# Optimization experiments

Measured on AMD Instinct MI355X. Metric: run time of the kernel, lower is better.

The kernel has to match this reference:

```python
import jax, jax.numpy as jnp
import numpy as np
import math

B, DG, P, DA = 512, 1024, 1024, 256
LN_EPS = 1e-5  # torch LayerNorm default
EPS = 1e-12


def _ln(x, g, b):
    mu = jnp.mean(x, axis=-1, keepdims=True)
    var = jnp.mean((x - mu) ** 2, axis=-1, keepdims=True)
    return (x - mu) * jax.lax.rsqrt(var + LN_EPS) * g + b


def setup_inputs() -> dict:
    key = jax.random.key(0)
    ks = jax.random.split(key, 16)
    s = lambda fan_in: 1.0 / math.sqrt(fan_in)
    return {
        "hg": jax.random.normal(ks[0], (B, DG), jnp.float32),
        "desc_2d": jax.random.normal(ks[1], (B, P), jnp.float32),
        "Wq": jax.random.uniform(ks[2], (DA, DG), jnp.float32, -s(DG), s(DG)),
        "bq": jnp.zeros((DA,), jnp.float32),
        "wk_val": jax.random.uniform(ks[3], (DA,), jnp.float32, -1.0, 1.0),
        "bk_val": jax.random.uniform(ks[4], (DA,), jnp.float32, -1.0, 1.0),
        "wv_val": jax.random.uniform(ks[5], (DA,), jnp.float32, -1.0, 1.0),
        "bv_val": jax.random.uniform(ks[6], (DA,), jnp.float32, -1.0, 1.0),
        "Ek": jax.random.normal(ks[7], (P, DA), jnp.float32),
        "Ev": jax.random.normal(ks[8], (P, DA), jnp.float32),
        "Uq": jax.random.uniform(ks[9], (DA, DA), jnp.float32, -s(DA), s(DA)),
        "Vk": jax.random.uniform(ks[10], (DA, DA), jnp.float32, -s(DA), s(DA)),
        "ln_q_g": jnp.ones((DA,), jnp.float32), "ln_q_b": jnp.zeros((DA,), jnp.float32),
        "ln_k_g": jnp.ones((DA,), jnp.float32), "ln_k_b": jnp.zeros((DA,), jnp.float32),
        "ln_v_g": jnp.ones((DA,), jnp.float32), "ln_v_b": jnp.zeros((DA,), jnp.float32),
    }


def reference(hg, desc_2d, Wq, bq, wk_val, bk_val, wv_val, bv_val, Ek, Ev, Uq, Vk,
              ln_q_g, ln_q_b, ln_k_g, ln_k_b, ln_v_g, ln_v_b):
    # dropout is inference-mode (identity)
    q = _ln(hg @ Wq.T + bq, ln_q_g, ln_q_b)                       # (B, DA)
    # scalar -> token proj plus id embedding
    k = desc_2d[:, :, None] * wk_val + bk_val + Ek[None]          # (B, P, DA)
    v = desc_2d[:, :, None] * wv_val + bv_val + Ev[None]
    k = _ln(k, ln_k_g, ln_k_b)
    v = _ln(v, ln_v_g, ln_v_b)
    q2 = q @ Uq.T                                                 # (B, DA)
    k2 = jnp.einsum('bpd,ed->bpe', k, Vk)                         # (B, P, DA)
    e = jnp.einsum('bpd,bd->bp', k2, q2) / math.sqrt(DA)          # (B, P)
    alpha = jax.nn.sigmoid(e)
    alpha = alpha / (jnp.sum(alpha, axis=1, keepdims=True) + EPS)
    c = jnp.einsum('bp,bpd->bd', alpha, v)                        # (B, DA)
    return c, alpha
```

## Files before the change

kernel.cpp:

```cpp
#include <hip/hip_runtime.h>
#include <math.h>

#define B 512
#define DG 1024
#define P 1024
#define DA 256
#define LDP 68
#define BP (B * P)
#define BD (B * DA)

__device__ __forceinline__ float block_reduce_sum(float v, volatile float* red) {
    #pragma unroll
    for (int off = 32; off > 0; off >>= 1) v += __shfl_down(v, off, 64);
    const int lane = threadIdx.x & 63, wid = threadIdx.x >> 6;
    __syncthreads();
    if (lane == 0) red[wid] = v;
    __syncthreads();
    return red[0] + red[1] + red[2] + red[3];
}
__device__ __forceinline__ float wsum(float v) {
    #pragma unroll
    for (int m = 32; m > 0; m >>= 1) v += __shfl_xor(v, m, 64);
    return v;
}

#define FMA16(a4, b4, acc)                                   \
    acc[0][0] = fmaf(a4.x, b4.x, acc[0][0]);                 \
    acc[0][1] = fmaf(a4.x, b4.y, acc[0][1]);                 \
    acc[0][2] = fmaf(a4.x, b4.z, acc[0][2]);                 \
    acc[0][3] = fmaf(a4.x, b4.w, acc[0][3]);                 \
    acc[1][0] = fmaf(a4.y, b4.x, acc[1][0]);                 \
    acc[1][1] = fmaf(a4.y, b4.y, acc[1][1]);                 \
    acc[1][2] = fmaf(a4.y, b4.z, acc[1][2]);                 \
    acc[1][3] = fmaf(a4.y, b4.w, acc[1][3]);                 \
    acc[2][0] = fmaf(a4.z, b4.x, acc[2][0]);                 \
    acc[2][1] = fmaf(a4.z, b4.y, acc[2][1]);                 \
    acc[2][2] = fmaf(a4.z, b4.z, acc[2][2]);                 \
    acc[2][3] = fmaf(a4.z, b4.w, acc[2][3]);                 \
    acc[3][0] = fmaf(a4.w, b4.x, acc[3][0]);                 \
    acc[3][1] = fmaf(a4.w, b4.y, acc[3][1]);                 \
    acc[3][2] = fmaf(a4.w, b4.z, acc[3][2]);                 \
    acc[3][3] = fmaf(a4.w, b4.w, acc[3][3]);

__device__ __forceinline__ void stage_T(const float* __restrict__ src, int ldk, int m0, int k0,
                                        int tid, float* sD) {
    const int m = tid >> 3, k4 = (tid & 7) * 4;
    #pragma unroll
    for (int pass = 0; pass < 2; ++pass) {
        int mm = m + pass * 32;
        float4 v = *reinterpret_cast<const float4*>(&src[(m0 + mm) * ldk + k0 + k4]);
        sD[(k4 + 0) * LDP + mm] = v.x; sD[(k4 + 1) * LDP + mm] = v.y;
        sD[(k4 + 2) * LDP + mm] = v.z; sD[(k4 + 3) * LDP + mm] = v.w;
    }
}
__device__ __forceinline__ void stage_N1(const float* __restrict__ src, int ldn, int k0, int n0,
                                         int tid, float* sD) {
    const int k = tid >> 4, n4 = (tid & 15) * 4;
    #pragma unroll
    for (int pass = 0; pass < 2; ++pass) {
        int kk = k + pass * 16;
        *reinterpret_cast<float4*>(&sD[kk * LDP + n4]) =
            *reinterpret_cast<const float4*>(&src[(k0 + kk) * ldn + n0 + n4]);
    }
}
__device__ __forceinline__ void stage_N2(const float* __restrict__ src, int pstride, int ldn,
                                         int k0, int n0, int tid, float* sD) {
    const int k = tid >> 4, n4 = (tid & 15) * 4;
    #pragma unroll
    for (int pass = 0; pass < 2; ++pass) {
        int kk = k + pass * 16;
        const float* base = &src[(k0 + kk) * ldn + n0 + n4];
        float4 v = *reinterpret_cast<const float4*>(base);
        float4 w = *reinterpret_cast<const float4*>(base + pstride);
        v.x += w.x; v.y += w.y; v.z += w.z; v.w += w.w;
        *reinterpret_cast<float4*>(&sD[kk * LDP + n4]) = v;
    }
}
__device__ __forceinline__ void mm_inner(const float* sA, const float* sB, int tid, float acc[4][4]) {
    const int ty4 = (tid >> 4) * 4, tx4 = (tid & 15) * 4;
    #pragma unroll
    for (int kk = 0; kk < 32; ++kk) {
        float4 a4 = *reinterpret_cast<const float4*>(&sA[kk * LDP + ty4]);
        float4 b4 = *reinterpret_cast<const float4*>(&sB[kk * LDP + tx4]);
        FMA16(a4, b4, acc)
    }
}

__global__ __launch_bounds__(256) void KA(const float* __restrict__ hg, const float* __restrict__ Wq,
                                          const float* __restrict__ Uq, const float* __restrict__ Vk,
                                          const float* __restrict__ Ek, const float* __restrict__ Ev,
                                          const float* __restrict__ wk, const float* __restrict__ bk,
                                          const float* __restrict__ wv, const float* __restrict__ bv,
                                          const float* __restrict__ gk, const float* __restrict__ bkln,
                                          float* __restrict__ qp, float* __restrict__ Gp,
                                          float* __restrict__ UqT,
                                          float* __restrict__ pst, float* __restrict__ scal4,
                                          float* __restrict__ vec4) {
    __shared__ __align__(16) float sA[32 * LDP];
    __shared__ __align__(16) float sB[32 * LDP];
    const int tid = threadIdx.x, t = blockIdx.x;
    const int ty4 = (tid >> 4) * 4, tx4 = (tid & 15) * 4;

    if (t < 256) {
        const int mt = t & 7, nt = (t >> 3) & 3, ks = t >> 5;
        const int b0 = mt * 64, d0 = nt * 64, kc = ks * 128;
        float acc[4][4] = {};
        for (int kt = 0; kt < 128; kt += 32) {
            stage_T(hg, DG, b0, kc + kt, tid, sA);
            stage_T(Wq, DG, d0, kc + kt, tid, sB);
            __syncthreads();
            mm_inner(sA, sB, tid, acc);
            __syncthreads();
        }
        float* outp = qp + ks * BD;
        #pragma unroll
        for (int i = 0; i < 4; ++i) {
            float4 o = make_float4(acc[i][0], acc[i][1], acc[i][2], acc[i][3]);
            *reinterpret_cast<float4*>(&outp[(b0 + ty4 + i) * DA + d0 + tx4]) = o;
        }
    } else if (t < 384) {
        const int t2 = t - 256;
        const int et = t2 & 3, pt = (t2 >> 2) & 15, ks = t2 >> 6;
        const int e0 = et * 64, p0 = pt * 64, kc = ks * 128;
        float acc[4][4] = {};
        for (int kt = 0; kt < 128; kt += 32) {
            const int kg = kc + kt;
            {
                const int m = tid >> 3, k4 = (tid & 7) * 4;
                float4 g = *reinterpret_cast<const float4*>(&gk[kg + k4]);
                #pragma unroll
                for (int pass = 0; pass < 2; ++pass) {
                    int mm = m + pass * 32;
                    float4 v = *reinterpret_cast<const float4*>(&Vk[(e0 + mm) * DA + kg + k4]);
                    sA[(k4 + 0) * LDP + mm] = v.x * g.x; sA[(k4 + 1) * LDP + mm] = v.y * g.y;
                    sA[(k4 + 2) * LDP + mm] = v.z * g.z; sA[(k4 + 3) * LDP + mm] = v.w * g.w;
                }
            }
            stage_T(Ek, DA, p0, kg, tid, sB);
            __syncthreads();
            mm_inner(sA, sB, tid, acc);
            __syncthreads();
        }
        float* outp = Gp + ks * (DA * P);
        #pragma unroll
        for (int i = 0; i < 4; ++i) {
            float4 o = make_float4(acc[i][0], acc[i][1], acc[i][2], acc[i][3]);
            *reinterpret_cast<float4*>(&outp[(e0 + ty4 + i) * P + p0 + tx4]) = o;
        }
    } else if (t < 448) {
        const int b2 = t - 384;
        const int e0 = (b2 & 7) * 32, f0 = (b2 >> 3) * 32;
        const int col = tid & 31, row8 = tid >> 5;
        #pragma unroll
        for (int pass = 0; pass < 4; ++pass) {
            int r = row8 + pass * 8;
            sA[r * 33 + col] = Uq[(e0 + r) * DA + f0 + col];
        }
        __syncthreads();
        #pragma unroll
        for (int pass = 0; pass < 4; ++pass) {
            int r = row8 + pass * 8;
            UqT[(f0 + r) * DA + e0 + col] = sA[col * 33 + r];
        }
    } else if (t == 448) {
        float* w4  = sA;
        float* tmp = sB;
        float gkd = gk[tid];
        w4[0 * 256 + tid] = wk[tid] * gkd;
        w4[1 * 256 + tid] = bk[tid] * gkd;
        w4[2 * 256 + tid] = gkd;
        w4[3 * 256 + tid] = bkln[tid];
        __syncthreads();
        const int dl = tid & 15, eg = tid >> 4;
        for (int eb = 0; eb < 16; ++eb) {
            int e = eb * 16 + eg;
            float p0 = 0.f, p1 = 0.f, p2 = 0.f, p3 = 0.f;
            #pragma unroll
            for (int tt = 0; tt < 16; ++tt) {
                int d = dl + tt * 16;
                float v = Vk[e * DA + d];
                p0 = fmaf(v, w4[d], p0);
                p1 = fmaf(v, w4[256 + d], p1);
                p2 = fmaf(v, w4[512 + d], p2);
                p3 = fmaf(v, w4[768 + d], p3);
            }
            #pragma unroll
            for (int m = 8; m > 0; m >>= 1) {
                p0 += __shfl_xor(p0, m, 16);
                p1 += __shfl_xor(p1, m, 16);
                p2 += __shfl_xor(p2, m, 16);
                p3 += __shfl_xor(p3, m, 16);
            }
            if (dl == 0) {
                tmp[e * 4 + 0] = p0; tmp[e * 4 + 1] = p1;
                tmp[e * 4 + 2] = p2; tmp[e * 4 + 3] = p3;
            }
        }
        __syncthreads();
        float a0 = 0.f, a1 = 0.f, a2 = 0.f, a3 = 0.f;
        for (int e = 0; e < 256; ++e) {
            float u = Uq[e * DA + tid];
            a0 = fmaf(u, tmp[e * 4 + 0], a0);
            a1 = fmaf(u, tmp[e * 4 + 1], a1);
            a2 = fmaf(u, tmp[e * 4 + 2], a2);
            a3 = fmaf(u, tmp[e * 4 + 3], a3);
        }
        vec4[tid] = a0; vec4[256 + tid] = a1; vec4[512 + tid] = a2; vec4[768 + tid] = a3;
    } else {
        const int tp = t - 449;
        const int wid = tid >> 6, lane = tid & 63;
        const int p = tp * 4 + wid;
        const int d4 = lane * 4;
        const float inv = 1.0f / DA;
        float4 ek4 = *reinterpret_cast<const float4*>(&Ek[p * DA + d4]);
        float4 ev4 = *reinterpret_cast<const float4*>(&Ev[p * DA + d4]);
        float4 wk4 = *reinterpret_cast<const float4*>(&wk[d4]);
        float4 bk4 = *reinterpret_cast<const float4*>(&bk[d4]);
        float4 wv4 = *reinterpret_cast<const float4*>(&wv[d4]);
        float4 bv4 = *reinterpret_cast<const float4*>(&bv[d4]);
        float ck0 = bk4.x + ek4.x, ck1 = bk4.y + ek4.y, ck2 = bk4.z + ek4.z, ck3 = bk4.w + ek4.w;
        float cv0 = bv4.x + ev4.x, cv1 = bv4.y + ev4.y, cv2 = bv4.z + ev4.z, cv3 = bv4.w + ev4.w;
        float Sck  = wsum(ck0 + ck1 + ck2 + ck3);
        float Sck2 = wsum(ck0*ck0 + ck1*ck1 + ck2*ck2 + ck3*ck3);
        float Swck = wsum(wk4.x*ck0 + wk4.y*ck1 + wk4.z*ck2 + wk4.w*ck3);
        float Scv  = wsum(cv0 + cv1 + cv2 + cv3);
        float Scv2 = wsum(cv0*cv0 + cv1*cv1 + cv2*cv2 + cv3*cv3);
        float Swcv = wsum(wv4.x*cv0 + wv4.y*cv1 + wv4.z*cv2 + wv4.w*cv3);
        float Swk  = wsum(wk4.x + wk4.y + wk4.z + wk4.w);
        float Swv  = wsum(wv4.x + wv4.y + wv4.z + wv4.w);
        float mwk = Swk * inv, mwv = Swv * inv;
        float mck = Sck * inv, mcv = Scv * inv;
        if (lane == 0) {
            pst[0 * P + p] = mck;
            pst[1 * P + p] = Swck * inv - mwk * mck;
            pst[2 * P + p] = Sck2 * inv - mck * mck;
            pst[3 * P + p] = mcv;
            pst[4 * P + p] = Swcv * inv - mwv * mcv;
            pst[5 * P + p] = Scv2 * inv - mcv * mcv;
        }
        if (p == 0) {
            float Swk2 = wsum(wk4.x*wk4.x + wk4.y*wk4.y + wk4.z*wk4.z + wk4.w*wk4.w);
            float Swv2 = wsum(wv4.x*wv4.x + wv4.y*wv4.y + wv4.z*wv4.z + wv4.w*wv4.w);
            if (lane == 0) {
                scal4[0] = mwk;
                scal4[1] = Swk2 * inv - mwk * mwk;
                scal4[2] = mwv;
                scal4[3] = Swv2 * inv - mwv * mwv;
            }
        }
    }
}

__global__ __launch_bounds__(256) void KC(const float* __restrict__ qp, const float* __restrict__ bq,
                                          const float* __restrict__ gq, const float* __restrict__ bqln,
                                          const float* __restrict__ vec4, const float* __restrict__ UqT,
                                          float* __restrict__ q2out, float* __restrict__ bscal) {
    __shared__ __align__(16) float q_lds[DA];
    __shared__ float red[4];
    const int b = blockIdx.x, d = threadIdx.x;
    float x = bq[d];
    #pragma unroll
    for (int ks = 0; ks < 8; ++ks) x += qp[ks * BD + b * DA + d];
    float mu = block_reduce_sum(x, red) * (1.0f / DA);
    float xc = x - mu;
    float var = block_reduce_sum(xc * xc, red) * (1.0f / DA);
    float qv = xc * rsqrtf(var + 1e-5f) * gq[d] + bqln[d];
    q_lds[d] = qv;
    float Wg = block_reduce_sum(qv * vec4[d], red);
    float Cg = block_reduce_sum(qv * vec4[256 + d], red);
    float G_ = block_reduce_sum(qv * vec4[512 + d], red);
    float Bb = block_reduce_sum(qv * vec4[768 + d], red);
    if (d == 0) {
        bscal[b] = Wg; bscal[B + b] = Cg;
        bscal[2 * B + b] = G_; bscal[3 * B + b] = Bb;
    }
    float q2 = 0.f;
    for (int f = 0; f < DA; f += 4) {
        float4 qf = *reinterpret_cast<const float4*>(&q_lds[f]);
        q2 = fmaf(qf.x, UqT[(f + 0) * DA + d], q2);
        q2 = fmaf(qf.y, UqT[(f + 1) * DA + d], q2);
        q2 = fmaf(qf.z, UqT[(f + 2) * DA + d], q2);
        q2 = fmaf(qf.w, UqT[(f + 3) * DA + d], q2);
    }
    q2out[b * DA + d] = q2;
}

__global__ __launch_bounds__(256) void KD(const float* __restrict__ q2, const float* __restrict__ Gp,
                                          float* __restrict__ epart) {
    __shared__ __align__(16) float sA[32 * LDP];
    __shared__ __align__(16) float sB[32 * LDP];
    const int tid = threadIdx.x, t = blockIdx.x;
    const int ty4 = (tid >> 4) * 4, tx4 = (tid & 15) * 4;
    const int bt = t & 7, pt = (t >> 3) & 15, ks = t >> 7;
    const int b0 = bt * 64, p0 = pt * 64, kc = ks * 64;
    float acc[4][4] = {};
    for (int kt = 0; kt < 64; kt += 32) {
        stage_T(q2, DA, b0, kc + kt, tid, sA);
        stage_N2(Gp, DA * P, P, kc + kt, p0, tid, sB);
        __syncthreads();
        mm_inner(sA, sB, tid, acc);
        __syncthreads();
    }
    float* outp = epart + ks * BP;
    #pragma unroll
    for (int i = 0; i < 4; ++i) {
        float4 o = make_float4(acc[i][0], acc[i][1], acc[i][2], acc[i][3]);
        *reinterpret_cast<float4*>(&outp[(b0 + ty4 + i) * P + p0 + tx4]) = o;
    }
}

__global__ __launch_bounds__(256) void KE(const float* __restrict__ epart, const float* __restrict__ desc,
                                          const float* __restrict__ bscal, const float* __restrict__ pst,
                                          const float* __restrict__ scal4,
                                          const float* __restrict__ gv, const float* __restrict__ wv,
                                          const float* __restrict__ bvv, const float* __restrict__ bvln,
                                          float* __restrict__ alpha_out, float* __restrict__ wbuf,
                                          float* __restrict__ bscal2, float* __restrict__ out_c) {
    __shared__ float red[4];
    const int b = blockIdx.x, tid = threadIdx.x;
    const float mwk = scal4[0], Ak = scal4[1], mwv = scal4[2], Av = scal4[3];
    const float Wg = bscal[b], Cg = bscal[B + b], G_ = bscal[2 * B + b], Bb = bscal[3 * B + b];
    float u[4];
    float us = 0.f, ws_ = 0.f, wss = 0.f, wms = 0.f;
    #pragma unroll
    for (int j = 0; j < 4; ++j) {
        int p = j * 256 + tid;
        float dot = epart[b * P + p] + epart[BP + b * P + p]
                  + epart[2 * BP + b * P + p] + epart[3 * BP + b * P + p];
        float s = desc[b * P + p];
        float mck = pst[p], Bk = pst[P + p], Ck = pst[2 * P + p];
        float var = fmaf(s, fmaf(s, Ak, 2.0f * Bk), Ck);
        float rstd = rsqrtf(var + 1e-5f);
        float mu = fmaf(s, mwk, mck);
        float e = (rstd * (fmaf(s, Wg, Cg) + dot - mu * G_) + Bb) * 0.0625f;
        float uu = 1.0f / (1.0f + expf(-e));
        float mcv = pst[3 * P + p], Bv = pst[4 * P + p], Cv = pst[5 * P + p];
        float varv = fmaf(s, fmaf(s, Av, 2.0f * Bv), Cv);
        float rv = rsqrtf(varv + 1e-5f);
        float ww = uu * rv;
        wbuf[b * P + p] = ww;
        u[j] = uu;
        us += uu; ws_ += ww;
        wss = fmaf(ww, s, wss);
        wms = fmaf(ww, fmaf(s, mwv, mcv), wms);
    }
    float S   = block_reduce_sum(us, red);
    float SB  = block_reduce_sum(ws_, red);
    float SBs = block_reduce_sum(wss, red);
    float SBm = block_reduce_sum(wms, red);
    float invS = 1.0f / (S + 1e-12f);
    float T = S * invS;
    #pragma unroll
    for (int j = 0; j < 4; ++j)
        alpha_out[b * P + j * 256 + tid] = u[j] * invS;
    if (tid == 0) bscal2[b] = invS;
    const int d = tid;
    out_c[b * DA + d] = invS * (gv[d] * (wv[d] * SBs + bvv[d] * SB - SBm)) + bvln[d] * T;
}

__global__ __launch_bounds__(256) void KF(const float* __restrict__ wbuf, const float* __restrict__ Ev,
                                          float* __restrict__ cpart) {
    __shared__ __align__(16) float sA[32 * LDP];
    __shared__ __align__(16) float sB[32 * LDP];
    const int tid = threadIdx.x, t = blockIdx.x;
    const int ty4 = (tid >> 4) * 4, tx4 = (tid & 15) * 4;
    const int mt = t & 7, nt = (t >> 3) & 3, ks = t >> 5;
    const int b0 = mt * 64, d0 = nt * 64, kc = ks * 64;
    float acc[4][4] = {};
    for (int kt = 0; kt < 64; kt += 32) {
        stage_T(wbuf, P, b0, kc + kt, tid, sA);
        stage_N1(Ev, DA, kc + kt, d0, tid, sB);
        __syncthreads();
        mm_inner(sA, sB, tid, acc);
        __syncthreads();
    }
    float* outp = cpart + ks * BD;
    #pragma unroll
    for (int i = 0; i < 4; ++i) {
        float4 o = make_float4(acc[i][0], acc[i][1], acc[i][2], acc[i][3]);
        *reinterpret_cast<float4*>(&outp[(b0 + ty4 + i) * DA + d0 + tx4]) = o;
    }
}

__global__ __launch_bounds__(256) void KG(const float* __restrict__ cpart, const float* __restrict__ bscal2,
                                          const float* __restrict__ gv, float* __restrict__ out_c) {
    const int b = blockIdx.x, d = threadIdx.x;
    float csum = 0.f;
    #pragma unroll
    for (int ks = 0; ks < 16; ++ks) csum += cpart[ks * BD + b * DA + d];
    out_c[b * DA + d] = fmaf(bscal2[b] * gv[d], csum, out_c[b * DA + d]);
}

extern "C" void kernel_launch(void* const* d_in, const int* in_sizes, int n_in,
                              void* d_out, int out_size, void* d_ws, size_t ws_size,
                              hipStream_t stream) {
    (void)in_sizes; (void)n_in; (void)out_size; (void)ws_size;
    const float* hg   = (const float*)d_in[0];
    const float* desc = (const float*)d_in[1];
    const float* Wq   = (const float*)d_in[2];
    const float* bq   = (const float*)d_in[3];
    const float* wk   = (const float*)d_in[4];
    const float* bk   = (const float*)d_in[5];
    const float* wv   = (const float*)d_in[6];
    const float* bv   = (const float*)d_in[7];
    const float* Ek   = (const float*)d_in[8];
    const float* Ev   = (const float*)d_in[9];
    const float* Uq   = (const float*)d_in[10];
    const float* Vk   = (const float*)d_in[11];
    const float* gq   = (const float*)d_in[12];
    const float* bqln = (const float*)d_in[13];
    const float* gk   = (const float*)d_in[14];
    const float* bkln = (const float*)d_in[15];
    const float* gv   = (const float*)d_in[16];
    const float* bvln = (const float*)d_in[17];

    float* out = (float*)d_out;
    float* out_c = out;
    float* out_alpha = out + BD;

    float* ws = (float*)d_ws;
    float* qp    = ws;
    float* Gp    = ws + 1048576;
    float* UqT   = ws + 1572864;
    float* q2    = ws + 1638400;
    float* epart = ws + 1769472;
    float* wbuf  = ws + 3866624;
    float* cpart = ws + 4390912;
    float* vec4  = ws + 6488064;
    float* bscal = ws + 6489088;
    float* bscal2= ws + 6491136;
    float* pst   = ws + 6491648;
    float* scal4 = ws + 6497792;

    KA<<<705, 256, 0, stream>>>(hg, Wq, Uq, Vk, Ek, Ev, wk, bk, wv, bv, gk, bkln,
                                qp, Gp, UqT, pst, scal4, vec4);
    KC<<<512, 256, 0, stream>>>(qp, bq, gq, bqln, vec4, UqT, q2, bscal);
    KD<<<512, 256, 0, stream>>>(q2, Gp, epart);
    KE<<<512, 256, 0, stream>>>(epart, desc, bscal, pst, scal4, gv, wv, bv, bvln,
                                out_alpha, wbuf, bscal2, out_c);
    KF<<<512, 256, 0, stream>>>(wbuf, Ev, cpart);
    KG<<<512, 256, 0, stream>>>(cpart, bscal2, gv, out_c);
}
```

Measured before the change: 64.05 us.

## Reassociate key projection through q2 and fuse sigmoid weights into context GEMM

```diff
diff --git a/kernel.cpp b/kernel.cpp
--- a/kernel.cpp
+++ b/kernel.cpp
@@ -63,19 +63,6 @@
             *reinterpret_cast<const float4*>(&src[(k0 + kk) * ldn + n0 + n4]);
     }
 }
-__device__ __forceinline__ void stage_N2(const float* __restrict__ src, int pstride, int ldn,
-                                         int k0, int n0, int tid, float* sD) {
-    const int k = tid >> 4, n4 = (tid & 15) * 4;
-    #pragma unroll
-    for (int pass = 0; pass < 2; ++pass) {
-        int kk = k + pass * 16;
-        const float* base = &src[(k0 + kk) * ldn + n0 + n4];
-        float4 v = *reinterpret_cast<const float4*>(base);
-        float4 w = *reinterpret_cast<const float4*>(base + pstride);
-        v.x += w.x; v.y += w.y; v.z += w.z; v.w += w.w;
-        *reinterpret_cast<float4*>(&sD[kk * LDP + n4]) = v;
-    }
-}
 __device__ __forceinline__ void mm_inner(const float* sA, const float* sB, int tid, float acc[4][4]) {
     const int ty4 = (tid >> 4) * 4, tx4 = (tid & 15) * 4;
     #pragma unroll
@@ -86,16 +73,28 @@
     }
 }
 
+__device__ __forceinline__ void epilog_uw(float dot, float s,
+                                          float mck, float Bk, float Ck,
+                                          float Bv, float Cv,
+                                          float mwk, float Ak, float Av,
+                                          float Wg, float Cg, float G_, float Bb,
+                                          float& u, float& w) {
+    float var = fmaf(s, fmaf(s, Ak, 2.0f * Bk), Ck);
+    float rstd = rsqrtf(var + 1e-5f);
+    float mu = fmaf(s, mwk, mck);
+    float e = (rstd * (fmaf(s, Wg, Cg) + dot - mu * G_) + Bb) * 0.0625f;
+    u = 1.0f / (1.0f + expf(-e));
+    float varv = fmaf(s, fmaf(s, Av, 2.0f * Bv), Cv);
+    w = u * rsqrtf(varv + 1e-5f);
+}
+
 __global__ __launch_bounds__(256) void KA(const float* __restrict__ hg, const float* __restrict__ Wq,
-                                          const float* __restrict__ Uq, const float* __restrict__ Vk,
+                                          const float* __restrict__ Uq,
                                           const float* __restrict__ Ek, const float* __restrict__ Ev,
                                           const float* __restrict__ wk, const float* __restrict__ bk,
                                           const float* __restrict__ wv, const float* __restrict__ bv,
-                                          const float* __restrict__ gk, const float* __restrict__ bkln,
-                                          float* __restrict__ qp, float* __restrict__ Gp,
-                                          float* __restrict__ UqT,
-                                          float* __restrict__ pst, float* __restrict__ scal4,
-                                          float* __restrict__ vec4) {
+                                          float* __restrict__ qp, float* __restrict__ UqT,
+                                          float* __restrict__ pst, float* __restrict__ scal4) {
     __shared__ __align__(16) float sA[32 * LDP];
     __shared__ __align__(16) float sB[32 * LDP];
     const int tid = threadIdx.x, t = blockIdx.x;
@@ -118,37 +117,8 @@
             float4 o = make_float4(acc[i][0], acc[i][1], acc[i][2], acc[i][3]);
             *reinterpret_cast<float4*>(&outp[(b0 + ty4 + i) * DA + d0 + tx4]) = o;
         }
-    } else if (t < 384) {
-        const int t2 = t - 256;
-        const int et = t2 & 3, pt = (t2 >> 2) & 15, ks = t2 >> 6;
-        const int e0 = et * 64, p0 = pt * 64, kc = ks * 128;
-        float acc[4][4] = {};
-        for (int kt = 0; kt < 128; kt += 32) {
-            const int kg = kc + kt;
-            {
-                const int m = tid >> 3, k4 = (tid & 7) * 4;
-                float4 g = *reinterpret_cast<const float4*>(&gk[kg + k4]);
-                #pragma unroll
-                for (int pass = 0; pass < 2; ++pass) {
-                    int mm = m + pass * 32;
-                    float4 v = *reinterpret_cast<const float4*>(&Vk[(e0 + mm) * DA + kg + k4]);
-                    sA[(k4 + 0) * LDP + mm] = v.x * g.x; sA[(k4 + 1) * LDP + mm] = v.y * g.y;
-                    sA[(k4 + 2) * LDP + mm] = v.z * g.z; sA[(k4 + 3) * LDP + mm] = v.w * g.w;
-                }
-            }
-            stage_T(Ek, DA, p0, kg, tid, sB);
-            __syncthreads();
-            mm_inner(sA, sB, tid, acc);
-            __syncthreads();
-        }
-        float* outp = Gp + ks * (DA * P);
-        #pragma unroll
-        for (int i = 0; i < 4; ++i) {
-            float4 o = make_float4(acc[i][0], acc[i][1], acc[i][2], acc[i][3]);
-            *reinterpret_cast<float4*>(&outp[(e0 + ty4 + i) * P + p0 + tx4]) = o;
-        }
-    } else if (t < 448) {
-        const int b2 = t - 384;
+    } else if (t < 320) {
+        const int b2 = t - 256;
         const int e0 = (b2 & 7) * 32, f0 = (b2 >> 3) * 32;
         const int col = tid & 31, row8 = tid >> 5;
         #pragma unroll
@@ -162,52 +132,8 @@
             int r = row8 + pass * 8;
             UqT[(f0 + r) * DA + e0 + col] = sA[col * 33 + r];
         }
-    } else if (t == 448) {
-        float* w4  = sA;
-        float* tmp = sB;
-        float gkd = gk[tid];
-        w4[0 * 256 + tid] = wk[tid] * gkd;
-        w4[1 * 256 + tid] = bk[tid] * gkd;
-        w4[2 * 256 + tid] = gkd;
-        w4[3 * 256 + tid] = bkln[tid];
-        __syncthreads();
-        const int dl = tid & 15, eg = tid >> 4;
-        for (int eb = 0; eb < 16; ++eb) {
-            int e = eb * 16 + eg;
-            float p0 = 0.f, p1 = 0.f, p2 = 0.f, p3 = 0.f;
-            #pragma unroll
-            for (int tt = 0; tt < 16; ++tt) {
-                int d = dl + tt * 16;
-                float v = Vk[e * DA + d];
-                p0 = fmaf(v, w4[d], p0);
-                p1 = fmaf(v, w4[256 + d], p1);
-                p2 = fmaf(v, w4[512 + d], p2);
-                p3 = fmaf(v, w4[768 + d], p3);
-            }
-            #pragma unroll
-            for (int m = 8; m > 0; m >>= 1) {
-                p0 += __shfl_xor(p0, m, 16);
-                p1 += __shfl_xor(p1, m, 16);
-                p2 += __shfl_xor(p2, m, 16);
-                p3 += __shfl_xor(p3, m, 16);
-            }
-            if (dl == 0) {
-                tmp[e * 4 + 0] = p0; tmp[e * 4 + 1] = p1;
-                tmp[e * 4 + 2] = p2; tmp[e * 4 + 3] = p3;
-            }
-        }
-        __syncthreads();
-        float a0 = 0.f, a1 = 0.f, a2 = 0.f, a3 = 0.f;
-        for (int e = 0; e < 256; ++e) {
-            float u = Uq[e * DA + tid];
-            a0 = fmaf(u, tmp[e * 4 + 0], a0);
-            a1 = fmaf(u, tmp[e * 4 + 1], a1);
-            a2 = fmaf(u, tmp[e * 4 + 2], a2);
-            a3 = fmaf(u, tmp[e * 4 + 3], a3);
-        }
-        vec4[tid] = a0; vec4[256 + tid] = a1; vec4[512 + tid] = a2; vec4[768 + tid] = a3;
     } else {
-        const int tp = t - 449;
+        const int tp = t - 320;
         const int wid = tid >> 6, lane = tid & 63;
         const int p = tp * 4 + wid;
         const int d4 = lane * 4;
@@ -253,9 +179,13 @@
 
 __global__ __launch_bounds__(256) void KC(const float* __restrict__ qp, const float* __restrict__ bq,
                                           const float* __restrict__ gq, const float* __restrict__ bqln,
-                                          const float* __restrict__ vec4, const float* __restrict__ UqT,
-                                          float* __restrict__ q2out, float* __restrict__ bscal) {
+                                          const float* __restrict__ UqT, const float* __restrict__ Vk,
+                                          const float* __restrict__ gk,
+                                          const float* __restrict__ wk, const float* __restrict__ bk,
+                                          const float* __restrict__ bkln,
+                                          float* __restrict__ gr, float* __restrict__ bscal) {
     __shared__ __align__(16) float q_lds[DA];
+    __shared__ __align__(16) float q2_lds[DA];
     __shared__ float red[4];
     const int b = blockIdx.x, d = threadIdx.x;
     float x = bq[d];
@@ -266,14 +196,8 @@
     float var = block_reduce_sum(xc * xc, red) * (1.0f / DA);
     float qv = xc * rsqrtf(var + 1e-5f) * gq[d] + bqln[d];
     q_lds[d] = qv;
-    float Wg = block_reduce_sum(qv * vec4[d], red);
-    float Cg = block_reduce_sum(qv * vec4[256 + d], red);
-    float G_ = block_reduce_sum(qv * vec4[512 + d], red);
-    float Bb = block_reduce_sum(qv * vec4[768 + d], red);
-    if (d == 0) {
-        bscal[b] = Wg; bscal[B + b] = Cg;
-        bscal[2 * B + b] = G_; bscal[3 * B + b] = Bb;
-    }
+    __syncthreads();
+
     float q2 = 0.f;
     for (int f = 0; f < DA; f += 4) {
         float4 qf = *reinterpret_cast<const float4*>(&q_lds[f]);
@@ -282,21 +206,42 @@
         q2 = fmaf(qf.z, UqT[(f + 2) * DA + d], q2);
         q2 = fmaf(qf.w, UqT[(f + 3) * DA + d], q2);
     }
-    q2out[b * DA + d] = q2;
-}
-
-__global__ __launch_bounds__(256) void KD(const float* __restrict__ q2, const float* __restrict__ Gp,
+    q2_lds[d] = q2;
+    __syncthreads();
+
+    float r = 0.f;
+    for (int e = 0; e < DA; e += 4) {
+        float4 qe = *reinterpret_cast<const float4*>(&q2_lds[e]);
+        r = fmaf(qe.x, Vk[(e + 0) * DA + d], r);
+        r = fmaf(qe.y, Vk[(e + 1) * DA + d], r);
+        r = fmaf(qe.z, Vk[(e + 2) * DA + d], r);
+        r = fmaf(qe.w, Vk[(e + 3) * DA + d], r);
+    }
+    float grv = gk[d] * r;
+    gr[b * DA + d] = grv;
+
+    float Wg = block_reduce_sum(wk[d] * grv, red);
+    float Cg = block_reduce_sum(bk[d] * grv, red);
+    float G_ = block_reduce_sum(grv, red);
+    float Bb = block_reduce_sum(bkln[d] * r, red);
+    if (d == 0) {
+        bscal[b] = Wg; bscal[B + b] = Cg;
+        bscal[2 * B + b] = G_; bscal[3 * B + b] = Bb;
+    }
+}
+
+__global__ __launch_bounds__(256) void KD(const float* __restrict__ gr, const float* __restrict__ Ek,
                                           float* __restrict__ epart) {
     __shared__ __align__(16) float sA[32 * LDP];
     __shared__ __align__(16) float sB[32 * LDP];
     const int tid = threadIdx.x, t = blockIdx.x;
     const int ty4 = (tid >> 4) * 4, tx4 = (tid & 15) * 4;
-    const int bt = t & 7, pt = (t >> 3) & 15, ks = t >> 7;
-    const int b0 = bt * 64, p0 = pt * 64, kc = ks * 64;
+    const int mt = t & 7, nt = (t >> 3) & 15, ks = t >> 7;
+    const int b0 = mt * 64, p0 = nt * 64, kc = ks * 128;
     float acc[4][4] = {};
-    for (int kt = 0; kt < 64; kt += 32) {
-        stage_T(q2, DA, b0, kc + kt, tid, sA);
-        stage_N2(Gp, DA * P, P, kc + kt, p0, tid, sB);
+    for (int kt = 0; kt < 128; kt += 32) {
+        stage_T(gr, DA, b0, kc + kt, tid, sA);
+        stage_T(Ek, DA, p0, kc + kt, tid, sB);
         __syncthreads();
         mm_inner(sA, sB, tid, acc);
         __syncthreads();
@@ -309,13 +254,69 @@
     }
 }
 
-__global__ __launch_bounds__(256) void KE(const float* __restrict__ epart, const float* __restrict__ desc,
+__global__ __launch_bounds__(256) void KF(const float* __restrict__ epart, const float* __restrict__ desc,
                                           const float* __restrict__ bscal, const float* __restrict__ pst,
-                                          const float* __restrict__ scal4,
+                                          const float* __restrict__ scal4, const float* __restrict__ Ev,
+                                          float* __restrict__ cpart) {
+    __shared__ __align__(16) float sA[32 * LDP];
+    __shared__ __align__(16) float sB[32 * LDP];
+    const int tid = threadIdx.x, t = blockIdx.x;
+    const int ty4 = (tid >> 4) * 4, tx4 = (tid & 15) * 4;
+    const int mt = t & 7, nt = (t >> 3) & 3, ks = t >> 5;
+    const int b0 = mt * 64, d0 = nt * 64, kc = ks * 128;
+    const float mwk = scal4[0], Ak = scal4[1], Av = scal4[3];
+    const int m = tid >> 3, k4 = (tid & 7) * 4;
+    float acc[4][4] = {};
+    for (int kt = 0; kt < 128; kt += 32) {
+        const int kg = kc + kt;
+        #pragma unroll
+        for (int pass = 0; pass < 2; ++pass) {
+            int mm = m + pass * 32;
+            const int b = b0 + mm;
+            const int p = kg + k4;
+            float4 e0 = *reinterpret_cast<const float4*>(&epart[b * P + p]);
+            float4 e1 = *reinterpret_cast<const float4*>(&epart[BP + b * P + p]);
+            float4 s4 = *reinterpret_cast<const float4*>(&desc[b * P + p]);
+            float4 mck4 = *reinterpret_cast<const float4*>(&pst[p]);
+            float4 Bk4  = *reinterpret_cast<const float4*>(&pst[P + p]);
+            float4 Ck4  = *reinterpret_cast<const float4*>(&pst[2 * P + p]);
+            float4 Bv4  = *reinterpret_cast<const float4*>(&pst[4 * P + p]);
+            float4 Cv4  = *reinterpret_cast<const float4*>(&pst[5 * P + p]);
+            const float Wg = bscal[b], Cg = bscal[B + b];
+            const float G_ = bscal[2 * B + b], Bb = bscal[3 * B + b];
+            float u, w;
+            epilog_uw(e0.x + e1.x, s4.x, mck4.x, Bk4.x, Ck4.x, Bv4.x, Cv4.x,
+                      mwk, Ak, Av, Wg, Cg, G_, Bb, u, w);
+            sA[(k4 + 0) * LDP + mm] = w;
+            epilog_uw(e0.y + e1.y, s4.y, mck4.y, Bk4.y, Ck4.y, Bv4.y, Cv4.y,
+                      mwk, Ak, Av, Wg, Cg, G_, Bb, u, w);
+            sA[(k4 + 1) * LDP + mm] = w;
+            epilog_uw(e0.z + e1.z, s4.z, mck4.z, Bk4.z, Ck4.z, Bv4.z, Cv4.z,
+                      mwk, Ak, Av, Wg, Cg, G_, Bb, u, w);
+            sA[(k4 + 2) * LDP + mm] = w;
+            epilog_uw(e0.w + e1.w, s4.w, mck4.w, Bk4.w, Ck4.w, Bv4.w, Cv4.w,
+                      mwk, Ak, Av, Wg, Cg, G_, Bb, u, w);
+            sA[(k4 + 3) * LDP + mm] = w;
+        }
+        stage_N1(Ev, DA, kg, d0, tid, sB);
+        __syncthreads();
+        mm_inner(sA, sB, tid, acc);
+        __syncthreads();
+    }
+    float* outp = cpart + ks * BD;
+    #pragma unroll
+    for (int i = 0; i < 4; ++i) {
+        float4 o = make_float4(acc[i][0], acc[i][1], acc[i][2], acc[i][3]);
+        *reinterpret_cast<float4*>(&outp[(b0 + ty4 + i) * DA + d0 + tx4]) = o;
+    }
+}
+
+__global__ __launch_bounds__(256) void KG(const float* __restrict__ epart, const float* __restrict__ desc,
+                                          const float* __restrict__ bscal, const float* __restrict__ pst,
+                                          const float* __restrict__ scal4, const float* __restrict__ cpart,
                                           const float* __restrict__ gv, const float* __restrict__ wv,
                                           const float* __restrict__ bvv, const float* __restrict__ bvln,
-                                          float* __restrict__ alpha_out, float* __restrict__ wbuf,
-                                          float* __restrict__ bscal2, float* __restrict__ out_c) {
+                                          float* __restrict__ alpha_out, float* __restrict__ out_c) {
     __shared__ float red[4];
     const int b = blockIdx.x, tid = threadIdx.x;
     const float mwk = scal4[0], Ak = scal4[1], mwv = scal4[2], Av = scal4[3];
@@ -325,24 +326,15 @@
     #pragma unroll
     for (int j = 0; j < 4; ++j) {
         int p = j * 256 + tid;
-        float dot = epart[b * P + p] + epart[BP + b * P + p]
-                  + epart[2 * BP + b * P + p] + epart[3 * BP + b * P + p];
+        float dot = epart[b * P + p] + epart[BP + b * P + p];
         float s = desc[b * P + p];
-        float mck = pst[p], Bk = pst[P + p], Ck = pst[2 * P + p];
-        float var = fmaf(s, fmaf(s, Ak, 2.0f * Bk), Ck);
-        float rstd = rsqrtf(var + 1e-5f);
-        float mu = fmaf(s, mwk, mck);
-        float e = (rstd * (fmaf(s, Wg, Cg) + dot - mu * G_) + Bb) * 0.0625f;
-        float uu = 1.0f / (1.0f + expf(-e));
-        float mcv = pst[3 * P + p], Bv = pst[4 * P + p], Cv = pst[5 * P + p];
-        float varv = fmaf(s, fmaf(s, Av, 2.0f * Bv), Cv);
-        float rv = rsqrtf(varv + 1e-5f);
-        float ww = uu * rv;
-        wbuf[b * P + p] = ww;
+        float uu, ww;
+        epilog_uw(dot, s, pst[p], pst[P + p], pst[2 * P + p], pst[4 * P + p], pst[5 * P + p],
+                  mwk, Ak, Av, Wg, Cg, G_, Bb, uu, ww);
         u[j] = uu;
         us += uu; ws_ += ww;
         wss = fmaf(ww, s, wss);
-        wms = fmaf(ww, fmaf(s, mwv, mcv), wms);
+        wms = fmaf(ww, fmaf(s, mwv, pst[3 * P + p]), wms);
     }
     float S   = block_reduce_sum(us, red);
     float SB  = block_reduce_sum(ws_, red);
@@ -353,42 +345,12 @@
     #pragma unroll
     for (int j = 0; j < 4; ++j)
         alpha_out[b * P + j * 256 + tid] = u[j] * invS;
-    if (tid == 0) bscal2[b] = invS;
     const int d = tid;
-    out_c[b * DA + d] = invS * (gv[d] * (wv[d] * SBs + bvv[d] * SB - SBm)) + bvln[d] * T;
-}
-
-__global__ __launch_bounds__(256) void KF(const float* __restrict__ wbuf, const float* __restrict__ Ev,
-                                          float* __restrict__ cpart) {
-    __shared__ __align__(16) float sA[32 * LDP];
-    __shared__ __align__(16) float sB[32 * LDP];
-    const int tid = threadIdx.x, t = blockIdx.x;
-    const int ty4 = (tid >> 4) * 4, tx4 = (tid & 15) * 4;
-    const int mt = t & 7, nt = (t >> 3) & 3, ks = t >> 5;
-    const int b0 = mt * 64, d0 = nt * 64, kc = ks * 64;
-    float acc[4][4] = {};
-    for (int kt = 0; kt < 64; kt += 32) {
-        stage_T(wbuf, P, b0, kc + kt, tid, sA);
-        stage_N1(Ev, DA, kc + kt, d0, tid, sB);
-        __syncthreads();
-        mm_inner(sA, sB, tid, acc);
-        __syncthreads();
-    }
-    float* outp = cpart + ks * BD;
-    #pragma unroll
-    for (int i = 0; i < 4; ++i) {
-        float4 o = make_float4(acc[i][0], acc[i][1], acc[i][2], acc[i][3]);
-        *reinterpret_cast<float4*>(&outp[(b0 + ty4 + i) * DA + d0 + tx4]) = o;
-    }
-}
-
-__global__ __launch_bounds__(256) void KG(const float* __restrict__ cpart, const float* __restrict__ bscal2,
-                                          const float* __restrict__ gv, float* __restrict__ out_c) {
-    const int b = blockIdx.x, d = threadIdx.x;
     float csum = 0.f;
     #pragma unroll
-    for (int ks = 0; ks < 16; ++ks) csum += cpart[ks * BD + b * DA + d];
-    out_c[b * DA + d] = fmaf(bscal2[b] * gv[d], csum, out_c[b * DA + d]);
+    for (int ks = 0; ks < 8; ++ks) csum += cpart[ks * BD + b * DA + d];
+    out_c[b * DA + d] =
+        invS * (gv[d] * (wv[d] * SBs + bvv[d] * SB + csum - SBm)) + bvln[d] * T;
 }
 
 extern "C" void kernel_launch(void* const* d_in, const int* in_sizes, int n_in,
@@ -420,24 +382,18 @@
 
     float* ws = (float*)d_ws;
     float* qp    = ws;
-    float* Gp    = ws + 1048576;
-    float* UqT   = ws + 1572864;
-    float* q2    = ws + 1638400;
-    float* epart = ws + 1769472;
-    float* wbuf  = ws + 3866624;
-    float* cpart = ws + 4390912;
-    float* vec4  = ws + 6488064;
-    float* bscal = ws + 6489088;
-    float* bscal2= ws + 6491136;
-    float* pst   = ws + 6491648;
-    float* scal4 = ws + 6497792;
-
-    KA<<<705, 256, 0, stream>>>(hg, Wq, Uq, Vk, Ek, Ev, wk, bk, wv, bv, gk, bkln,
-                                qp, Gp, UqT, pst, scal4, vec4);
-    KC<<<512, 256, 0, stream>>>(qp, bq, gq, bqln, vec4, UqT, q2, bscal);
-    KD<<<512, 256, 0, stream>>>(q2, Gp, epart);
-    KE<<<512, 256, 0, stream>>>(epart, desc, bscal, pst, scal4, gv, wv, bv, bvln,
-                                out_alpha, wbuf, bscal2, out_c);
-    KF<<<512, 256, 0, stream>>>(wbuf, Ev, cpart);
-    KG<<<512, 256, 0, stream>>>(cpart, bscal2, gv, out_c);
-}
+    float* UqT   = ws + 1048576;
+    float* gr    = ws + 1114112;
+    float* epart = ws + 1245184;
+    float* cpart = ws + 2293760;
+    float* bscal = ws + 3342336;
+    float* pst   = ws + 3344384;
+    float* scal4 = ws + 3350528;
+
+    KA<<<576, 256, 0, stream>>>(hg, Wq, Uq, Ek, Ev, wk, bk, wv, bv, qp, UqT, pst, scal4);
+    KC<<<512, 256, 0, stream>>>(qp, bq, gq, bqln, UqT, Vk, gk, wk, bk, bkln, gr, bscal);
+    KD<<<256, 256, 0, stream>>>(gr, Ek, epart);
+    KF<<<256, 256, 0, stream>>>(epart, desc, bscal, pst, scal4, Ev, cpart);
+    KG<<<512, 256, 0, stream>>>(epart, desc, bscal, pst, scal4, cpart, gv, wv, bv, bvln,
+                                out_alpha, out_c);
+}
```

After: 57.52 us (median of 2 runs). -10.2%, faster.
